# Kernel optimization log

Hardware: AMD Instinct MI355X
Metric: run time of the kernel (lower is better)

Reference implementation:

```python
import jax, jax.numpy as jnp
import numpy as np

EPS = 1e-5

def _conv1x1(x, w, b=None):
    # x: (B, Cin, H, W), w: (Cout, Cin) -> (B, Cout, H, W)
    y = jnp.einsum('bchw,oc->bohw', x, w)
    if b is not None:
        y = y + b[None, :, None, None]
    return y

def setup_inputs() -> dict:
    key = jax.random.key(0)
    ks = jax.random.split(key, 14)
    B, C, I = 4, 256, 128
    Ha = Wa = 64
    Hd = Wd = 128
    s = 0.05
    return {
        'detect':  jax.random.normal(ks[0], (B, C, Hd, Wd), jnp.float32),
        'aim':     jax.random.normal(ks[1], (B, C, Ha, Wa), jnp.float32),
        'g_w':     jax.random.normal(ks[2], (I, C), jnp.float32) * s,
        'g_b':     jax.random.normal(ks[3], (I,), jnp.float32) * s,
        'theta_w': jax.random.normal(ks[4], (I, C), jnp.float32) * s,
        'theta_b': jax.random.normal(ks[5], (I,), jnp.float32) * s,
        'phi_w':   jax.random.normal(ks[6], (I, C), jnp.float32) * s,
        'phi_b':   jax.random.normal(ks[7], (I,), jnp.float32) * s,
        'q_w':     jax.random.normal(ks[8], (C, I), jnp.float32) * s,
        'q_b':     jax.random.normal(ks[9], (C,), jnp.float32) * s,
        'bn_gamma': jax.random.normal(ks[10], (C,), jnp.float32),
        'bn_beta':  jax.random.normal(ks[11], (C,), jnp.float32),
        'bn_mean':  jax.random.normal(ks[12], (C,), jnp.float32),
        'bn_var':   jax.random.uniform(ks[13], (C,), jnp.float32) + 0.5,
    }

def reference(detect, aim, g_w, g_b, theta_w, theta_b, phi_w, phi_b,
              q_w, q_b, bn_gamma, bn_beta, bn_mean, bn_var):
    B, C, Hd, Wd = detect.shape
    _, _, Ha, Wa = aim.shape
    Na = Ha * Wa
    Nd = Hd * Wd
    I = g_w.shape[0]

    # 1x1 conv projections, flattened to token sequences
    a_g   = _conv1x1(aim, g_w, g_b).reshape(B, I, Na)        # g(aim)
    th_a  = _conv1x1(aim, theta_w, theta_b).reshape(B, I, Na)
    ph_d  = _conv1x1(detect, phi_w, phi_b).reshape(B, I, Nd)
    # (d_x = g(detect) is dead code in the original forward; omitted)

    # f = theta_x @ phi_x : (B, Na, Nd); permuted -> (B, Nd, Na); N = Na
    f = jnp.einsum('bia,bid->bad', th_a, ph_d)               # (B, Na, Nd)
    inv_n = jnp.float32(1.0 / Na)
    # non_det = (f^T / Na) @ a_x : (B, Nd, I) -> permute -> (B, I, Nd)
    non = jnp.einsum('bad,bia->bid', f * inv_n, a_g)         # (B, I, Nd)
    non = non.reshape(B, I, Hd, Wd)

    # Q: 1x1 conv (I -> C) + BatchNorm (inference mode, running stats)
    y = _conv1x1(non, q_w, q_b)
    inv_std = jax.lax.rsqrt(bn_var + EPS)
    y = (y - bn_mean[None, :, None, None]) * (bn_gamma * inv_std)[None, :, None, None] \
        + bn_beta[None, :, None, None]

    return y + detect
```

## Files before the change

### kernel.cpp

```cpp
#include <hip/hip_runtime.h>
#include <hip/hip_cooperative_groups.h>

namespace cg = cooperative_groups;

constexpr int BB   = 4;
constexpr int CCH  = 256;
constexpr int IDIM = 128;
constexpr int NAa  = 4096;
constexpr int NDd  = 16384;
constexpr int PAD  = 320;
constexpr float NAinv = 1.0f / 4096.0f;

typedef __bf16 bf16x8 __attribute__((ext_vector_type(8)));
typedef float  f32x4  __attribute__((ext_vector_type(4)));

__device__ inline unsigned short f2bfu(float f) {
    unsigned u = __float_as_uint(f);
    u += 0x7FFFu + ((u >> 16) & 1u);
    return (unsigned short)(u >> 16);
}

struct Par {
    const float* aim; const float* qw; const float* gw; const float* gb;
    const float* thw; const float* thb; const float* phw; const float* phb;
    const float* qb; const float* gamma; const float* beta; const float* mean; const float* var;
    const float* detect; float* out;
    unsigned short* Abf; float* r; float* Spart;
    unsigned short* Shat; unsigned short* Ph; unsigned short* Rt; unsigned short* Th; unsigned short* W5;
    float* b5;
};

template<int PHASE> __device__ inline void gsync() {
    if constexpr (PHASE < 0) cg::this_grid().sync();
}

template<int PHASE>
__global__ __launch_bounds__(512, 4) void k_mega(Par p) {
    __shared__ __align__(16) char smraw[32768];
    const int bid = blockIdx.x, t = threadIdx.x;
    const int wv = t >> 6, lane = t & 63, quad = lane >> 4, l16 = lane & 15;

    if (PHASE < 0 || PHASE == 0) {
        {
            const int half = t >> 8, tt = t & 255;
            const int row = bid * 2 + half;
            const float* src = p.aim + (long)row * NAa;
            unsigned short* dst = p.Abf + (long)row * NAa;
            float s = 0.f;
            #pragma unroll
            for (int j = 0; j < 4; ++j) {
                const int e = (j * 256 + tt) * 4;
                float4 v = *(const float4*)(src + e);
                s += v.x + v.y + v.z + v.w;
                ushort4 o; o.x = f2bfu(v.x); o.y = f2bfu(v.y); o.z = f2bfu(v.z); o.w = f2bfu(v.w);
                *(ushort4*)(dst + e) = o;
            }
            float* red = (float*)smraw;
            red[t] = s; __syncthreads();
            for (int st_ = 128; st_ > 0; st_ >>= 1) {
                if (tt < st_) red[half * 256 + tt] += red[half * 256 + tt + st_];
                __syncthreads();
            }
            if (tt == 0) p.r[row] = red[half * 256];
        }
        {
            const int idx = bid * 512 + t;
            if (idx < CCH * PAD) {
                const int o = idx / PAD, c = idx - o * PAD;
                float acc = 0.f;
                if (c <= 256) {
                    for (int i = 0; i < IDIM; ++i)
                        acc += p.qw[o * IDIM + i] * ((c < 256) ? p.gw[i * CCH + c] : p.gb[i]);
                }
                p.Ph[idx] = f2bfu(acc);
            } else if (idx < CCH * PAD + PAD * PAD) {
                const int id2 = idx - CCH * PAD;
                const int c2 = id2 / PAD, k = id2 - c2 * PAD;
                float acc = 0.f;
                if (k <= 256 && c2 <= 256) {
                    for (int i = 0; i < IDIM; ++i) {
                        const float av = (k < 256) ? p.thw[i * CCH + k] : p.thb[i];
                        const float bv = (c2 < 256) ? p.phw[i * CCH + c2] : p.phb[i];
                        acc += av * bv;
                    }
                }
                p.Rt[id2] = f2bfu(acc);
            }
        }
    }
    gsync<PHASE>();

    if (PHASE < 0 || PHASE == 1) {
        const int z = bid >> 4, rem = bid & 15;
        const int b = z >> 3;
        const unsigned short* A = p.Abf + (long)b * CCH * NAa;
        const int mb = (rem >> 2) * 64, nbb = (rem & 3) * 64;
        const int kb = (z & 7) * 512;
        f32x4 acc[4][4] = {};
        #pragma unroll
        for (int s = 0; s < 2; ++s) {
            const int k = kb + (wv * 2 + s) * 32 + quad * 8;
            bf16x8 af[4], bfr[4];
            #pragma unroll
            for (int i = 0; i < 4; ++i) af[i]  = *(const bf16x8*)(A + (long)(mb + i * 16 + l16) * NAa + k);
            #pragma unroll
            for (int j = 0; j < 4; ++j) bfr[j] = *(const bf16x8*)(A + (long)(nbb + j * 16 + l16) * NAa + k);
            #pragma unroll
            for (int i = 0; i < 4; ++i)
                #pragma unroll
                for (int j = 0; j < 4; ++j)
                    acc[i][j] = __builtin_amdgcn_mfma_f32_16x16x32_bf16(af[i], bfr[j], acc[i][j], 0, 0, 0);
        }
        float* sred = (float*)smraw;
        auto lput = [&](int rg) {
            #pragma unroll
            for (int i = 0; i < 4; ++i)
                #pragma unroll
                for (int j = 0; j < 4; ++j)
                    #pragma unroll
                    for (int rr = 0; rr < 4; ++rr)
                        sred[rg * 4096 + ((i * 4 + j) * 4 + rr) * 64 + lane] = acc[i][j][rr];
        };
        auto ladd = [&](int rg) {
            #pragma unroll
            for (int i = 0; i < 4; ++i)
                #pragma unroll
                for (int j = 0; j < 4; ++j)
                    #pragma unroll
                    for (int rr = 0; rr < 4; ++rr)
                        acc[i][j][rr] += sred[rg * 4096 + ((i * 4 + j) * 4 + rr) * 64 + lane];
        };
        if (wv == 4 || wv == 5) lput(wv - 4);
        __syncthreads();
        if (wv == 0 || wv == 1) ladd(wv);
        __syncthreads();
        if (wv == 6 || wv == 7) lput(wv - 6);
        __syncthreads();
        if (wv == 2 || wv == 3) ladd(wv - 2);
        __syncthreads();
        if (wv == 2 || wv == 3) lput(wv - 2);
        __syncthreads();
        if (wv == 0 || wv == 1) ladd(wv);
        __syncthreads();
        if (wv == 1) lput(0);
        __syncthreads();
        if (wv == 0) {
            ladd(0);
            float* o = p.Spart + (long)z * CCH * CCH;
            #pragma unroll
            for (int i = 0; i < 4; ++i)
                #pragma unroll
                for (int j = 0; j < 4; ++j)
                    #pragma unroll
                    for (int reg = 0; reg < 4; ++reg)
                        o[(long)(mb + i * 16 + quad * 4 + reg) * CCH + nbb + j * 16 + l16] = acc[i][j][reg];
        }
    }
    gsync<PHASE>();

    if (PHASE < 0 || PHASE == 2) {
        for (int e = bid * 512 + t; e < BB * PAD * PAD; e += 512 * 512) {
            const int b = e / (PAD * PAD), idx = e - b * (PAD * PAD);
            const int k = idx / PAD, n = idx - k * PAD;
            float v = 0.f;
            if (k < 256 && n < 256) {
                #pragma unroll
                for (int pp = 0; pp < 8; ++pp)
                    v += p.Spart[(long)(b * 8 + pp) * CCH * CCH + k * CCH + n];
            } else if (k == 256 && n < 256) v = p.r[b * CCH + n];
            else if (n == 256 && k < 256)   v = p.r[b * CCH + k];
            else if (k == 256 && n == 256)  v = 4096.0f;
            p.Shat[(long)b * PAD * PAD + idx] = f2bfu(v);
        }
    }
    gsync<PHASE>();

    if (PHASE < 0 || PHASE == 3) {
        if (wv == 0 && (bid % 6) == 0 && (bid / 6) < 80) {
            const int tid = bid / 6;
            const int b = tid / 20, rem2 = tid % 20;
            const int n0 = (rem2 % 5) * 64, m0 = (rem2 / 5) * 64;
            const unsigned short* S = p.Shat + (long)b * PAD * PAD;
            unsigned short* T = p.Th + (long)b * CCH * PAD;
            f32x4 acc[4][4] = {};
            for (int kt = 0; kt < PAD; kt += 32) {
                bf16x8 af[4], bfr[4];
                #pragma unroll
                for (int i = 0; i < 4; ++i) af[i]  = *(const bf16x8*)(p.Ph + (long)(m0 + i * 16 + l16) * PAD + kt + quad * 8);
                #pragma unroll
                for (int j = 0; j < 4; ++j) bfr[j] = *(const bf16x8*)(S + (long)(n0 + j * 16 + l16) * PAD + kt + quad * 8);
                #pragma unroll
                for (int i = 0; i < 4; ++i)
                    #pragma unroll
                    for (int j = 0; j < 4; ++j)
                        acc[i][j] = __builtin_amdgcn_mfma_f32_16x16x32_bf16(af[i], bfr[j], acc[i][j], 0, 0, 0);
            }
            #pragma unroll
            for (int i = 0; i < 4; ++i)
                #pragma unroll
                for (int j = 0; j < 4; ++j)
                    #pragma unroll
                    for (int reg = 0; reg < 4; ++reg)
                        T[(long)(m0 + i * 16 + quad * 4 + reg) * PAD + n0 + j * 16 + l16] = f2bfu(acc[i][j][reg]);
        }
    }
    gsync<PHASE>();

    if (PHASE < 0 || PHASE == 4) {
        if (wv == 0 && (bid % 6) == 0 && (bid / 6) < 80) {
            const int tid = bid / 6;
            const int b = tid / 20, rem2 = tid % 20;
            const int n0 = (rem2 % 5) * 64, m0 = (rem2 / 5) * 64;
            const unsigned short* A = p.Th + (long)b * CCH * PAD;
            f32x4 acc[4][4] = {};
            for (int kt = 0; kt < PAD; kt += 32) {
                bf16x8 af[4], bfr[4];
                #pragma unroll
                for (int i = 0; i < 4; ++i) af[i]  = *(const bf16x8*)(A + (long)(m0 + i * 16 + l16) * PAD + kt + quad * 8);
                #pragma unroll
                for (int j = 0; j < 4; ++j) bfr[j] = *(const bf16x8*)(p.Rt + (long)(n0 + j * 16 + l16) * PAD + kt + quad * 8);
                #pragma unroll
                for (int i = 0; i < 4; ++i)
                    #pragma unroll
                    for (int j = 0; j < 4; ++j)
                        acc[i][j] = __builtin_amdgcn_mfma_f32_16x16x32_bf16(af[i], bfr[j], acc[i][j], 0, 0, 0);
            }
            #pragma unroll
            for (int i = 0; i < 4; ++i) {
                #pragma unroll
                for (int reg = 0; reg < 4; ++reg) {
                    const int o = m0 + i * 16 + quad * 4 + reg;
                    const float s = p.gamma[o] * rsqrtf(p.var[o] + 1e-5f);
                    #pragma unroll
                    for (int j = 0; j < 4; ++j) {
                        const int c2 = n0 + j * 16 + l16;
                        const float val = acc[i][j][reg] * s * NAinv;
                        if (c2 < CCH)
                            p.W5[((long)b * CCH + o) * CCH + c2] = f2bfu(val + (o == c2 ? 1.0f : 0.0f));
                        else if (c2 == CCH)
                            p.b5[b * CCH + o] = val + s * (p.qb[o] - p.mean[o]) + p.beta[o];
                    }
                }
            }
        }
    }
    gsync<PHASE>();

    if (PHASE < 0 || PHASE == 5) {
        const int z = bid >> 7;
        const int nb = (bid & 127) * 128;
        const float* D = p.detect + (long)z * CCH * NDd;
        float* O = p.out + (long)z * CCH * NDd;
        const unsigned short* W = p.W5 + (long)z * CCH * CCH;
        const int mw = (wv >> 1) * 64, nw = (wv & 1) * 64;
        const int r2 = t >> 4, g = t & 15;
        const bool st = (t < 256);
        auto lb = (unsigned short (*)[128][40])smraw;

        f32x4 xa[4], xb[4];
        bf16x8 af2[2][4], bfr[4];

        auto load_tile = [&](f32x4* x, int kt) {
            const float* base = D + (long)(kt + 2 * r2) * NDd + nb + 8 * g;
            x[0] = *(const f32x4*)(base);
            x[1] = *(const f32x4*)(base + NDd);
            x[2] = *(const f32x4*)(base + 4);
            x[3] = *(const f32x4*)(base + NDd + 4);
        };
        auto write_tile = [&](int buf, const f32x4* x) {
            #pragma unroll
            for (int e2 = 0; e2 < 2; ++e2)
                #pragma unroll
                for (int c = 0; c < 4; ++c) {
                    const int n = 8 * g + 4 * e2 + c;
                    const int pp = ((n & 7) << 4) + (n >> 3);
                    const unsigned v = (unsigned)f2bfu(x[2 * e2][c]) |
                                       ((unsigned)f2bfu(x[2 * e2 + 1][c]) << 16);
                    *(unsigned*)&lb[buf][pp][2 * r2] = v;
                }
        };
        auto loadW = [&](bf16x8* a, int kt) {
            #pragma unroll
            for (int i = 0; i < 4; ++i)
                a[i] = *(const bf16x8*)(W + (long)(mw + i * 16 + l16) * CCH + kt + quad * 8);
        };

        int pj[4];
        #pragma unroll
        for (int j = 0; j < 4; ++j) {
            const int n = nw + j * 16 + l16;
            pj[j] = ((n & 7) << 4) + (n >> 3);
        }

        f32x4 acc[4][4] = {};
        __syncthreads();
        if (st) { load_tile(xa, 0); load_tile(xb, 32); }
        loadW(af2[0], 0);
        if (st) { write_tile(0, xa); load_tile(xa, 64); }
        #pragma unroll
        for (int it = 0; it < 8; ++it) {
            __syncthreads();
            const int kt = it * 32;
            #pragma unroll
            for (int j = 0; j < 4; ++j)
                bfr[j] = *(const bf16x8*)&lb[it & 1][pj[j]][quad * 8];
            #pragma unroll
            for (int i = 0; i < 4; ++i)
                #pragma unroll
                for (int j = 0; j < 4; ++j)
                    acc[i][j] = __builtin_amdgcn_mfma_f32_16x16x32_bf16(af2[it & 1][i], bfr[j], acc[i][j], 0, 0, 0);
            if (it < 7) {
                loadW(af2[(it + 1) & 1], kt + 32);
                if (st) {
                    write_tile((it + 1) & 1, (it & 1) ? xa : xb);
                    if (it < 5) load_tile((it & 1) ? xa : xb, (it + 3) * 32);
                }
            }
        }
        #pragma unroll
        for (int i = 0; i < 4; ++i) {
            float bv[4];
            #pragma unroll
            for (int reg = 0; reg < 4; ++reg)
                bv[reg] = p.b5[z * CCH + mw + i * 16 + quad * 4 + reg];
            #pragma unroll
            for (int j = 0; j < 4; ++j) {
                const int n = nb + nw + j * 16 + l16;
                #pragma unroll
                for (int reg = 0; reg < 4; ++reg)
                    O[(long)(mw + i * 16 + quad * 4 + reg) * NDd + n] = acc[i][j][reg] + bv[reg];
            }
        }
    }
}

extern "C" void kernel_launch(void* const* d_in, const int* in_sizes, int n_in,
                              void* d_out, int out_size, void* d_ws, size_t ws_size,
                              hipStream_t stream) {
    float* ws = (float*)d_ws;
    unsigned short* Abf = (unsigned short*)ws;
    float* r     = ws + 2097152;
    float* Spart = r + 1024;
    unsigned short* ub = (unsigned short*)(Spart + 2097152);
    unsigned short* Shat_u  = ub;
    unsigned short* Phat_u  = Shat_u + 409600;
    unsigned short* RhatT_u = Phat_u + 81920;
    unsigned short* That_u  = RhatT_u + 102400;
    unsigned short* W5u     = That_u + 327680;
    float* b5 = (float*)(W5u + 262144);

    Par pp;
    pp.aim    = (const float*)d_in[1];
    pp.qw     = (const float*)d_in[8];
    pp.gw     = (const float*)d_in[2];
    pp.gb     = (const float*)d_in[3];
    pp.thw    = (const float*)d_in[4];
    pp.thb    = (const float*)d_in[5];
    pp.phw    = (const float*)d_in[6];
    pp.phb    = (const float*)d_in[7];
    pp.qb     = (const float*)d_in[9];
    pp.gamma  = (const float*)d_in[10];
    pp.beta   = (const float*)d_in[11];
    pp.mean   = (const float*)d_in[12];
    pp.var    = (const float*)d_in[13];
    pp.detect = (const float*)d_in[0];
    pp.out    = (float*)d_out;
    pp.Abf = Abf; pp.r = r; pp.Spart = Spart;
    pp.Shat = Shat_u; pp.Ph = Phat_u; pp.Rt = RhatT_u; pp.Th = That_u; pp.W5 = W5u;
    pp.b5 = b5;

    static int occ = -1;
    if (occ < 0) {
        if (hipOccupancyMaxActiveBlocksPerMultiprocessor(&occ, k_mega<-1>, 512, 0) != hipSuccess)
            occ = 0;
    }
    if (occ >= 2) {
        void* args[] = { (void*)&pp };
        hipLaunchCooperativeKernel(k_mega<-1>, dim3(512), dim3(512), args, 0, stream);
    } else {
        k_mega<0><<<dim3(512), dim3(512), 0, stream>>>(pp);
        k_mega<1><<<dim3(512), dim3(512), 0, stream>>>(pp);
        k_mega<2><<<dim3(512), dim3(512), 0, stream>>>(pp);
        k_mega<3><<<dim3(512), dim3(512), 0, stream>>>(pp);
        k_mega<4><<<dim3(512), dim3(512), 0, stream>>>(pp);
        k_mega<5><<<dim3(512), dim3(512), 0, stream>>>(pp);
    }
}
```

Baseline: 252.9 us.

## Halve cooperative grid to 256 blocks with two tasks per block per phase

Shrinks the cooperative mega-kernel grid from 512 to 256 blocks (one per CU), relaxes launch bounds to 2 blocks/CU, and has each block loop over two work items in the conversion, Gram and output phases. The small T/R GEMM phases are retiled to 32-row tiles so 160 consecutive blocks share the work instead of every sixth block. The aim is cheaper grid-wide barriers and more registers per thread, at the cost of less parallelism to hide latency in the bandwidth-heavy output phase.

```diff
diff --git a/kernel.cpp b/kernel.cpp
--- a/kernel.cpp
+++ b/kernel.cpp
@@ -10,6 +10,7 @@
 constexpr int NDd  = 16384;
 constexpr int PAD  = 320;
 constexpr float NAinv = 1.0f / 4096.0f;
+constexpr int NBLK = 256;
 
 typedef __bf16 bf16x8 __attribute__((ext_vector_type(8)));
 typedef float  f32x4  __attribute__((ext_vector_type(4)));
@@ -35,7 +36,7 @@
 }
 
 template<int PHASE>
-__global__ __launch_bounds__(512, 4) void k_mega(Par p) {
+__global__ __launch_bounds__(512, 2) void k_mega(Par p) {
     __shared__ __align__(16) char smraw[32768];
     const int bid = blockIdx.x, t = threadIdx.x;
     const int wv = t >> 6, lane = t & 63, quad = lane >> 4, l16 = lane & 15;
@@ -43,28 +44,31 @@
     if (PHASE < 0 || PHASE == 0) {
         {
             const int half = t >> 8, tt = t & 255;
-            const int row = bid * 2 + half;
-            const float* src = p.aim + (long)row * NAa;
-            unsigned short* dst = p.Abf + (long)row * NAa;
-            float s = 0.f;
-            #pragma unroll
-            for (int j = 0; j < 4; ++j) {
-                const int e = (j * 256 + tt) * 4;
-                float4 v = *(const float4*)(src + e);
-                s += v.x + v.y + v.z + v.w;
-                ushort4 o; o.x = f2bfu(v.x); o.y = f2bfu(v.y); o.z = f2bfu(v.z); o.w = f2bfu(v.w);
-                *(ushort4*)(dst + e) = o;
-            }
             float* red = (float*)smraw;
-            red[t] = s; __syncthreads();
-            for (int st_ = 128; st_ > 0; st_ >>= 1) {
-                if (tt < st_) red[half * 256 + tt] += red[half * 256 + tt + st_];
+            #pragma unroll
+            for (int rr = 0; rr < 2; ++rr) {
+                const int row = bid * 4 + half * 2 + rr;
+                const float* src = p.aim + (long)row * NAa;
+                unsigned short* dst = p.Abf + (long)row * NAa;
+                float s = 0.f;
+                #pragma unroll
+                for (int j = 0; j < 4; ++j) {
+                    const int e = (j * 256 + tt) * 4;
+                    float4 v = *(const float4*)(src + e);
+                    s += v.x + v.y + v.z + v.w;
+                    ushort4 o; o.x = f2bfu(v.x); o.y = f2bfu(v.y); o.z = f2bfu(v.z); o.w = f2bfu(v.w);
+                    *(ushort4*)(dst + e) = o;
+                }
                 __syncthreads();
-            }
-            if (tt == 0) p.r[row] = red[half * 256];
-        }
-        {
-            const int idx = bid * 512 + t;
+                red[t] = s; __syncthreads();
+                for (int st_ = 128; st_ > 0; st_ >>= 1) {
+                    if (tt < st_) red[half * 256 + tt] += red[half * 256 + tt + st_];
+                    __syncthreads();
+                }
+                if (tt == 0) p.r[row] = red[half * 256];
+            }
+        }
+        for (int idx = bid * 512 + t; idx < CCH * PAD + PAD * PAD; idx += NBLK * 512) {
             if (idx < CCH * PAD) {
                 const int o = idx / PAD, c = idx - o * PAD;
                 float acc = 0.f;
@@ -73,7 +77,7 @@
                         acc += p.qw[o * IDIM + i] * ((c < 256) ? p.gw[i * CCH + c] : p.gb[i]);
                 }
                 p.Ph[idx] = f2bfu(acc);
-            } else if (idx < CCH * PAD + PAD * PAD) {
+            } else {
                 const int id2 = idx - CCH * PAD;
                 const int c2 = id2 / PAD, k = id2 - c2 * PAD;
                 float acc = 0.f;
@@ -91,75 +95,80 @@
     gsync<PHASE>();
 
     if (PHASE < 0 || PHASE == 1) {
-        const int z = bid >> 4, rem = bid & 15;
-        const int b = z >> 3;
-        const unsigned short* A = p.Abf + (long)b * CCH * NAa;
-        const int mb = (rem >> 2) * 64, nbb = (rem & 3) * 64;
-        const int kb = (z & 7) * 512;
-        f32x4 acc[4][4] = {};
+        float* sred = (float*)smraw;
         #pragma unroll
-        for (int s = 0; s < 2; ++s) {
-            const int k = kb + (wv * 2 + s) * 32 + quad * 8;
-            bf16x8 af[4], bfr[4];
-            #pragma unroll
-            for (int i = 0; i < 4; ++i) af[i]  = *(const bf16x8*)(A + (long)(mb + i * 16 + l16) * NAa + k);
-            #pragma unroll
-            for (int j = 0; j < 4; ++j) bfr[j] = *(const bf16x8*)(A + (long)(nbb + j * 16 + l16) * NAa + k);
-            #pragma unroll
-            for (int i = 0; i < 4; ++i)
-                #pragma unroll
-                for (int j = 0; j < 4; ++j)
-                    acc[i][j] = __builtin_amdgcn_mfma_f32_16x16x32_bf16(af[i], bfr[j], acc[i][j], 0, 0, 0);
-        }
-        float* sred = (float*)smraw;
-        auto lput = [&](int rg) {
-            #pragma unroll
-            for (int i = 0; i < 4; ++i)
-                #pragma unroll
-                for (int j = 0; j < 4; ++j)
-                    #pragma unroll
-                    for (int rr = 0; rr < 4; ++rr)
-                        sred[rg * 4096 + ((i * 4 + j) * 4 + rr) * 64 + lane] = acc[i][j][rr];
-        };
-        auto ladd = [&](int rg) {
-            #pragma unroll
-            for (int i = 0; i < 4; ++i)
-                #pragma unroll
-                for (int j = 0; j < 4; ++j)
-                    #pragma unroll
-                    for (int rr = 0; rr < 4; ++rr)
-                        acc[i][j][rr] += sred[rg * 4096 + ((i * 4 + j) * 4 + rr) * 64 + lane];
-        };
-        if (wv == 4 || wv == 5) lput(wv - 4);
-        __syncthreads();
-        if (wv == 0 || wv == 1) ladd(wv);
-        __syncthreads();
-        if (wv == 6 || wv == 7) lput(wv - 6);
-        __syncthreads();
-        if (wv == 2 || wv == 3) ladd(wv - 2);
-        __syncthreads();
-        if (wv == 2 || wv == 3) lput(wv - 2);
-        __syncthreads();
-        if (wv == 0 || wv == 1) ladd(wv);
-        __syncthreads();
-        if (wv == 1) lput(0);
-        __syncthreads();
-        if (wv == 0) {
-            ladd(0);
-            float* o = p.Spart + (long)z * CCH * CCH;
-            #pragma unroll
-            for (int i = 0; i < 4; ++i)
-                #pragma unroll
-                for (int j = 0; j < 4; ++j)
-                    #pragma unroll
-                    for (int reg = 0; reg < 4; ++reg)
-                        o[(long)(mb + i * 16 + quad * 4 + reg) * CCH + nbb + j * 16 + l16] = acc[i][j][reg];
+        for (int s2 = 0; s2 < 2; ++s2) {
+            const int task = s2 * NBLK + bid;
+            const int z = task >> 4, rem = task & 15;
+            const int b = z >> 3;
+            const unsigned short* A = p.Abf + (long)b * CCH * NAa;
+            const int mb = (rem >> 2) * 64, nbb = (rem & 3) * 64;
+            const int kb = (z & 7) * 512;
+            f32x4 acc[4][4] = {};
+            #pragma unroll
+            for (int s = 0; s < 2; ++s) {
+                const int k = kb + (wv * 2 + s) * 32 + quad * 8;
+                bf16x8 af[4], bfr[4];
+                #pragma unroll
+                for (int i = 0; i < 4; ++i) af[i]  = *(const bf16x8*)(A + (long)(mb + i * 16 + l16) * NAa + k);
+                #pragma unroll
+                for (int j = 0; j < 4; ++j) bfr[j] = *(const bf16x8*)(A + (long)(nbb + j * 16 + l16) * NAa + k);
+                #pragma unroll
+                for (int i = 0; i < 4; ++i)
+                    #pragma unroll
+                    for (int j = 0; j < 4; ++j)
+                        acc[i][j] = __builtin_amdgcn_mfma_f32_16x16x32_bf16(af[i], bfr[j], acc[i][j], 0, 0, 0);
+            }
+            auto lput = [&](int rg) {
+                #pragma unroll
+                for (int i = 0; i < 4; ++i)
+                    #pragma unroll
+                    for (int j = 0; j < 4; ++j)
+                        #pragma unroll
+                        for (int rr = 0; rr < 4; ++rr)
+                            sred[rg * 4096 + ((i * 4 + j) * 4 + rr) * 64 + lane] = acc[i][j][rr];
+            };
+            auto ladd = [&](int rg) {
+                #pragma unroll
+                for (int i = 0; i < 4; ++i)
+                    #pragma unroll
+                    for (int j = 0; j < 4; ++j)
+                        #pragma unroll
+                        for (int rr = 0; rr < 4; ++rr)
+                            acc[i][j][rr] += sred[rg * 4096 + ((i * 4 + j) * 4 + rr) * 64 + lane];
+            };
+            __syncthreads();
+            if (wv == 4 || wv == 5) lput(wv - 4);
+            __syncthreads();
+            if (wv == 0 || wv == 1) ladd(wv);
+            __syncthreads();
+            if (wv == 6 || wv == 7) lput(wv - 6);
+            __syncthreads();
+            if (wv == 2 || wv == 3) ladd(wv - 2);
+            __syncthreads();
+            if (wv == 2 || wv == 3) lput(wv - 2);
+            __syncthreads();
+            if (wv == 0 || wv == 1) ladd(wv);
+            __syncthreads();
+            if (wv == 1) lput(0);
+            __syncthreads();
+            if (wv == 0) {
+                ladd(0);
+                float* o = p.Spart + (long)z * CCH * CCH;
+                #pragma unroll
+                for (int i = 0; i < 4; ++i)
+                    #pragma unroll
+                    for (int j = 0; j < 4; ++j)
+                        #pragma unroll
+                        for (int reg = 0; reg < 4; ++reg)
+                            o[(long)(mb + i * 16 + quad * 4 + reg) * CCH + nbb + j * 16 + l16] = acc[i][j][reg];
+            }
         }
     }
     gsync<PHASE>();
 
     if (PHASE < 0 || PHASE == 2) {
-        for (int e = bid * 512 + t; e < BB * PAD * PAD; e += 512 * 512) {
+        for (int e = bid * 512 + t; e < BB * PAD * PAD; e += NBLK * 512) {
             const int b = e / (PAD * PAD), idx = e - b * (PAD * PAD);
             const int k = idx / PAD, n = idx - k * PAD;
             float v = 0.f;
@@ -176,27 +185,26 @@
     gsync<PHASE>();
 
     if (PHASE < 0 || PHASE == 3) {
-        if (wv == 0 && (bid % 6) == 0 && (bid / 6) < 80) {
-            const int tid = bid / 6;
-            const int b = tid / 20, rem2 = tid % 20;
-            const int n0 = (rem2 % 5) * 64, m0 = (rem2 / 5) * 64;
+        if (wv == 0 && bid < 160) {
+            const int b = bid / 40, rem2 = bid % 40;
+            const int m0 = (rem2 / 5) * 32, n0 = (rem2 % 5) * 64;
             const unsigned short* S = p.Shat + (long)b * PAD * PAD;
             unsigned short* T = p.Th + (long)b * CCH * PAD;
-            f32x4 acc[4][4] = {};
+            f32x4 acc[2][4] = {};
             for (int kt = 0; kt < PAD; kt += 32) {
-                bf16x8 af[4], bfr[4];
-                #pragma unroll
-                for (int i = 0; i < 4; ++i) af[i]  = *(const bf16x8*)(p.Ph + (long)(m0 + i * 16 + l16) * PAD + kt + quad * 8);
+                bf16x8 af[2], bfr[4];
+                #pragma unroll
+                for (int i = 0; i < 2; ++i) af[i]  = *(const bf16x8*)(p.Ph + (long)(m0 + i * 16 + l16) * PAD + kt + quad * 8);
                 #pragma unroll
                 for (int j = 0; j < 4; ++j) bfr[j] = *(const bf16x8*)(S + (long)(n0 + j * 16 + l16) * PAD + kt + quad * 8);
                 #pragma unroll
-                for (int i = 0; i < 4; ++i)
+                for (int i = 0; i < 2; ++i)
                     #pragma unroll
                     for (int j = 0; j < 4; ++j)
                         acc[i][j] = __builtin_amdgcn_mfma_f32_16x16x32_bf16(af[i], bfr[j], acc[i][j], 0, 0, 0);
             }
             #pragma unroll
-            for (int i = 0; i < 4; ++i)
+            for (int i = 0; i < 2; ++i)
                 #pragma unroll
                 for (int j = 0; j < 4; ++j)
                     #pragma unroll
@@ -207,26 +215,25 @@
     gsync<PHASE>();
 
     if (PHASE < 0 || PHASE == 4) {
-        if (wv == 0 && (bid % 6) == 0 && (bid / 6) < 80) {
-            const int tid = bid / 6;
-            const int b = tid / 20, rem2 = tid % 20;
-            const int n0 = (rem2 % 5) * 64, m0 = (rem2 / 5) * 64;
+        if (wv == 0 && bid < 160) {
+            const int b = bid / 40, rem2 = bid % 40;
+            const int m0 = (rem2 / 5) * 32, n0 = (rem2 % 5) * 64;
             const unsigned short* A = p.Th + (long)b * CCH * PAD;
-            f32x4 acc[4][4] = {};
+            f32x4 acc[2][4] = {};
             for (int kt = 0; kt < PAD; kt += 32) {
-                bf16x8 af[4], bfr[4];
-                #pragma unroll
-                for (int i = 0; i < 4; ++i) af[i]  = *(const bf16x8*)(A + (long)(m0 + i * 16 + l16) * PAD + kt + quad * 8);
+                bf16x8 af[2], bfr[4];
+                #pragma unroll
+                for (int i = 0; i < 2; ++i) af[i]  = *(const bf16x8*)(A + (long)(m0 + i * 16 + l16) * PAD + kt + quad * 8);
                 #pragma unroll
                 for (int j = 0; j < 4; ++j) bfr[j] = *(const bf16x8*)(p.Rt + (long)(n0 + j * 16 + l16) * PAD + kt + quad * 8);
                 #pragma unroll
-                for (int i = 0; i < 4; ++i)
+                for (int i = 0; i < 2; ++i)
                     #pragma unroll
                     for (int j = 0; j < 4; ++j)
                         acc[i][j] = __builtin_amdgcn_mfma_f32_16x16x32_bf16(af[i], bfr[j], acc[i][j], 0, 0, 0);
             }
             #pragma unroll
-            for (int i = 0; i < 4; ++i) {
+            for (int i = 0; i < 2; ++i) {
                 #pragma unroll
                 for (int reg = 0; reg < 4; ++reg) {
                     const int o = m0 + i * 16 + quad * 4 + reg;
@@ -247,43 +254,10 @@
     gsync<PHASE>();
 
     if (PHASE < 0 || PHASE == 5) {
-        const int z = bid >> 7;
-        const int nb = (bid & 127) * 128;
-        const float* D = p.detect + (long)z * CCH * NDd;
-        float* O = p.out + (long)z * CCH * NDd;
-        const unsigned short* W = p.W5 + (long)z * CCH * CCH;
         const int mw = (wv >> 1) * 64, nw = (wv & 1) * 64;
         const int r2 = t >> 4, g = t & 15;
         const bool st = (t < 256);
         auto lb = (unsigned short (*)[128][40])smraw;
-
-        f32x4 xa[4], xb[4];
-        bf16x8 af2[2][4], bfr[4];
-
-        auto load_tile = [&](f32x4* x, int kt) {
-            const float* base = D + (long)(kt + 2 * r2) * NDd + nb + 8 * g;
-            x[0] = *(const f32x4*)(base);
-            x[1] = *(const f32x4*)(base + NDd);
-            x[2] = *(const f32x4*)(base + 4);
-            x[3] = *(const f32x4*)(base + NDd + 4);
-        };
-        auto write_tile = [&](int buf, const f32x4* x) {
-            #pragma unroll
-            for (int e2 = 0; e2 < 2; ++e2)
-                #pragma unroll
-                for (int c = 0; c < 4; ++c) {
-                    const int n = 8 * g + 4 * e2 + c;
-                    const int pp = ((n & 7) << 4) + (n >> 3);
-                    const unsigned v = (unsigned)f2bfu(x[2 * e2][c]) |
-                                       ((unsigned)f2bfu(x[2 * e2 + 1][c]) << 16);
-                    *(unsigned*)&lb[buf][pp][2 * r2] = v;
-                }
-        };
-        auto loadW = [&](bf16x8* a, int kt) {
-            #pragma unroll
-            for (int i = 0; i < 4; ++i)
-                a[i] = *(const bf16x8*)(W + (long)(mw + i * 16 + l16) * CCH + kt + quad * 8);
-        };
 
         int pj[4];
         #pragma unroll
@@ -292,43 +266,81 @@
             pj[j] = ((n & 7) << 4) + (n >> 3);
         }
 
-        f32x4 acc[4][4] = {};
-        __syncthreads();
-        if (st) { load_tile(xa, 0); load_tile(xb, 32); }
-        loadW(af2[0], 0);
-        if (st) { write_tile(0, xa); load_tile(xa, 64); }
         #pragma unroll
-        for (int it = 0; it < 8; ++it) {
-            __syncthreads();
-            const int kt = it * 32;
-            #pragma unroll
-            for (int j = 0; j < 4; ++j)
-                bfr[j] = *(const bf16x8*)&lb[it & 1][pj[j]][quad * 8];
-            #pragma unroll
-            for (int i = 0; i < 4; ++i)
+        for (int s2 = 0; s2 < 2; ++s2) {
+            const int task = s2 * NBLK + bid;
+            const int z = task >> 7;
+            const int nb = (task & 127) * 128;
+            const float* D = p.detect + (long)z * CCH * NDd;
+            float* O = p.out + (long)z * CCH * NDd;
+            const unsigned short* W = p.W5 + (long)z * CCH * CCH;
+
+            f32x4 xa[4], xb[4];
+            bf16x8 af2[2][4], bfr[4];
+
+            auto load_tile = [&](f32x4* x, int kt) {
+                const float* base = D + (long)(kt + 2 * r2) * NDd + nb + 8 * g;
+                x[0] = *(const f32x4*)(base);
+                x[1] = *(const f32x4*)(base + NDd);
+                x[2] = *(const f32x4*)(base + 4);
+                x[3] = *(const f32x4*)(base + NDd + 4);
+            };
+            auto write_tile = [&](int buf, const f32x4* x) {
+                #pragma unroll
+                for (int e2 = 0; e2 < 2; ++e2)
+                    #pragma unroll
+                    for (int c = 0; c < 4; ++c) {
+                        const int n = 8 * g + 4 * e2 + c;
+                        const int pp = ((n & 7) << 4) + (n >> 3);
+                        const unsigned v = (unsigned)f2bfu(x[2 * e2][c]) |
+                                           ((unsigned)f2bfu(x[2 * e2 + 1][c]) << 16);
+                        *(unsigned*)&lb[buf][pp][2 * r2] = v;
+                    }
+            };
+            auto loadW = [&](bf16x8* a, int kt) {
+                #pragma unroll
+                for (int i = 0; i < 4; ++i)
+                    a[i] = *(const bf16x8*)(W + (long)(mw + i * 16 + l16) * CCH + kt + quad * 8);
+            };
+
+            f32x4 acc[4][4] = {};
+            __syncthreads();
+            if (st) { load_tile(xa, 0); load_tile(xb, 32); }
+            loadW(af2[0], 0);
+            if (st) { write_tile(0, xa); load_tile(xa, 64); }
+            #pragma unroll
+            for (int it = 0; it < 8; ++it) {
+                __syncthreads();
+                const int kt = it * 32;
                 #pragma unroll
                 for (int j = 0; j < 4; ++j)
-                    acc[i][j] = __builtin_amdgcn_mfma_f32_16x16x32_bf16(af2[it & 1][i], bfr[j], acc[i][j], 0, 0, 0);
-            if (it < 7) {
-                loadW(af2[(it + 1) & 1], kt + 32);
-                if (st) {
-                    write_tile((it + 1) & 1, (it & 1) ? xa : xb);
-                    if (it < 5) load_tile((it & 1) ? xa : xb, (it + 3) * 32);
-                }
-            }
-        }
-        #pragma unroll
-        for (int i = 0; i < 4; ++i) {
-            float bv[4];
-            #pragma unroll
-            for (int reg = 0; reg < 4; ++reg)
-                bv[reg] = p.b5[z * CCH + mw + i * 16 + quad * 4 + reg];
-            #pragma unroll
-            for (int j = 0; j < 4; ++j) {
-                const int n = nb + nw + j * 16 + l16;
+                    bfr[j] = *(const bf16x8*)&lb[it & 1][pj[j]][quad * 8];
+                #pragma unroll
+                for (int i = 0; i < 4; ++i)
+                    #pragma unroll
+                    for (int j = 0; j < 4; ++j)
+                        acc[i][j] = __builtin_amdgcn_mfma_f32_16x16x32_bf16(af2[it & 1][i], bfr[j], acc[i][j], 0, 0, 0);
+                if (it < 7) {
+                    loadW(af2[(it + 1) & 1], kt + 32);
+                    if (st) {
+                        write_tile((it + 1) & 1, (it & 1) ? xa : xb);
+                        if (it < 5) load_tile((it & 1) ? xa : xb, (it + 3) * 32);
+                    }
+                }
+            }
+            #pragma unroll
+            for (int i = 0; i < 4; ++i) {
+                float bv[4];
                 #pragma unroll
                 for (int reg = 0; reg < 4; ++reg)
-                    O[(long)(mw + i * 16 + quad * 4 + reg) * NDd + n] = acc[i][j][reg] + bv[reg];
+                    bv[reg] = p.b5[z * CCH + mw + i * 16 + quad * 4 + reg];
+                #pragma unroll
+                for (int j = 0; j < 4; ++j) {
+                    const int n = nb + nw + j * 16 + l16;
+                    #pragma unroll
+                    for (int reg = 0; reg < 4; ++reg)
+                        O[(long)(mw + i * 16 + quad * 4 + reg) * NDd + n] = acc[i][j][reg] + bv[reg];
+                }
             }
         }
     }
@@ -374,15 +386,15 @@
         if (hipOccupancyMaxActiveBlocksPerMultiprocessor(&occ, k_mega<-1>, 512, 0) != hipSuccess)
             occ = 0;
     }
-    if (occ >= 2) {
+    if (occ >= 1) {
         void* args[] = { (void*)&pp };
-        hipLaunchCooperativeKernel(k_mega<-1>, dim3(512), dim3(512), args, 0, stream);
+        hipLaunchCooperativeKernel(k_mega<-1>, dim3(NBLK), dim3(512), args, 0, stream);
     } else {
-        k_mega<0><<<dim3(512), dim3(512), 0, stream>>>(pp);
-        k_mega<1><<<dim3(512), dim3(512), 0, stream>>>(pp);
-        k_mega<2><<<dim3(512), dim3(512), 0, stream>>>(pp);
-        k_mega<3><<<dim3(512), dim3(512), 0, stream>>>(pp);
-        k_mega<4><<<dim3(512), dim3(512), 0, stream>>>(pp);
-        k_mega<5><<<dim3(512), dim3(512), 0, stream>>>(pp);
+        k_mega<0><<<dim3(NBLK), dim3(512), 0, stream>>>(pp);
+        k_mega<1><<<dim3(NBLK), dim3(512), 0, stream>>>(pp);
+        k_mega<2><<<dim3(NBLK), dim3(512), 0, stream>>>(pp);
+        k_mega<3><<<dim3(NBLK), dim3(512), 0, stream>>>(pp);
+        k_mega<4><<<dim3(NBLK), dim3(512), 0, stream>>>(pp);
+        k_mega<5><<<dim3(NBLK), dim3(512), 0, stream>>>(pp);
     }
 }
```

New measurement: 232.0 us. 8.3% less time.
